# Optimization experiments

Hardware: AMD Instinct MI355X
Metric: run time of the kernel (lower is better)

Reference implementation:

```python
import jax, jax.numpy as jnp
import numpy as np

B, T, D = 8, 1024, 1024

def setup_inputs() -> dict:
    key = jax.random.key(0)
    ks = jax.random.split(key, 9)
    s = D ** -0.5
    return {
        "x": jax.random.normal(ks[0], (B, T, D), dtype=jnp.float32),
        "w_q": jax.random.normal(ks[1], (D, D), dtype=jnp.float32) * s,
        "b_q": jax.random.normal(ks[2], (D,), dtype=jnp.float32) * 0.02,
        "w_k": jax.random.normal(ks[3], (D, D), dtype=jnp.float32) * s,
        "b_k": jax.random.normal(ks[4], (D,), dtype=jnp.float32) * 0.02,
        "w_v": jax.random.normal(ks[5], (D, D), dtype=jnp.float32) * s,
        "b_v": jax.random.normal(ks[6], (D,), dtype=jnp.float32) * 0.02,
        "w_o": jax.random.normal(ks[7], (D, D), dtype=jnp.float32) * s,
        "b_o": jax.random.normal(ks[8], (D,), dtype=jnp.float32) * 0.02,
    }

def reference(x, w_q, b_q, w_k, b_k, w_v, b_v, w_o, b_o):
    d = x.shape[-1]
    scale = jnp.asarray(d, x.dtype) ** -0.5
    q = jnp.einsum('btd,ed->bte', x, w_q) + b_q  # nn.Linear: x @ W^T + b
    k = jnp.einsum('btd,ed->bte', x, w_k) + b_k
    v = jnp.einsum('btd,ed->bte', x, w_v) + b_v
    t = x.shape[1]
    causal = jnp.tril(jnp.ones((t, t), dtype=bool))  # (T, T)
    scores = jnp.einsum('bqd,bkd->bqk', q, k) * scale
    scores = jnp.where(causal, scores, -jnp.inf)
    attn = jax.nn.softmax(scores, axis=-1)  # max-subtraction folded in
    out = jnp.einsum('bqk,bkd->bqd', attn, v)
    return jnp.einsum('btd,ed->bte', out, w_o) + b_o
```

## Files before the change

kernel.cpp:

```cpp
#include <hip/hip_runtime.h>

typedef unsigned short u16;
typedef __attribute__((ext_vector_type(8))) short short8;
typedef __attribute__((ext_vector_type(4))) float f32x4;


__device__ __forceinline__ u16 f2bf(float f) {
  unsigned u = __builtin_bit_cast(unsigned, f);
  u += 0x7fffu + ((u >> 16) & 1u);
  return (u16)(u >> 16);
}

__device__ __forceinline__ void gload16(const void* g, void* l) {
  __builtin_amdgcn_global_load_lds(
      (const __attribute__((address_space(1))) unsigned*)g,
      (__attribute__((address_space(3))) unsigned*)l, 16, 0, 0);
}

__device__ __forceinline__ void gemm_tile(
    const u16* __restrict__ A, int lda,
    const u16* __restrict__ B, int ldb,
    int m0, int n0, int kend,
    char* sA, char* sB, f32x4 acc[4][4])
{
  const int tid  = threadIdx.x;
  const int lane = tid & 63;
  const int wave = tid >> 6;
  const int quad = lane >> 4;
  const int l16  = lane & 15;
  const int wr   = (wave >> 1) << 6;
  const int wc   = (wave & 1) << 6;

  const u16* ga[4]; const u16* gb[4]; int lb[4];
#pragma unroll
  for (int j = 0; j < 4; ++j) {
    const int Lb = j * 256 + wave * 64;
    const int L  = Lb + lane;
    const int r  = L >> 3;
    const int c  = (L & 7) ^ (r & 7);
    lb[j] = Lb * 16;
    ga[j] = A + (size_t)(m0 + r) * lda + c * 8;
    gb[j] = B + (size_t)(n0 + r) * ldb + c * 8;
  }

  for (int kt = 0; kt < kend; kt += 64) {
#pragma unroll
    for (int j = 0; j < 4; ++j) {
      gload16(ga[j], sA + lb[j]);
      gload16(gb[j], sB + lb[j]);
      ga[j] += 64; gb[j] += 64;
    }
    __syncthreads();
#pragma unroll
    for (int kk = 0; kk < 2; ++kk) {
      short8 af[4], bfr[4];
#pragma unroll
      for (int i = 0; i < 4; ++i) {
        const int rm = wr + i * 16 + l16;
        af[i]  = *(const short8*)(sA + rm * 128 + (((kk << 2) + quad) ^ (rm & 7)) * 16);
        const int rn = wc + i * 16 + l16;
        bfr[i] = *(const short8*)(sB + rn * 128 + (((kk << 2) + quad) ^ (rn & 7)) * 16);
      }
#pragma unroll
      for (int i = 0; i < 4; ++i)
#pragma unroll
        for (int j = 0; j < 4; ++j)
          acc[i][j] = __builtin_amdgcn_mfma_f32_16x16x32_bf16(af[i], bfr[j], acc[i][j], 0, 0, 0);
    }
    __syncthreads();
  }
}

__device__ __forceinline__ void gemm_tile_64(
    const u16* __restrict__ A, int lda,
    const u16* __restrict__ B, int ldb,
    int m0, int n0, int kend,
    char* sA, char* sB, f32x4 acc[2][4])
{
  const int tid  = threadIdx.x;
  const int lane = tid & 63;
  const int wave = tid >> 6;
  const int quad = lane >> 4;
  const int l16  = lane & 15;
  const int wr   = (wave >> 1) << 5;
  const int wc   = (wave & 1) << 6;

  const u16* ga[2]; int la[2];
  const u16* gb[4]; int lb[4];
#pragma unroll
  for (int j = 0; j < 2; ++j) {
    const int Lb = j * 256 + wave * 64;
    const int L  = Lb + lane;
    const int r  = L >> 3;
    const int c  = (L & 7) ^ (r & 7);
    la[j] = Lb * 16;
    ga[j] = A + (size_t)(m0 + r) * lda + c * 8;
  }
#pragma unroll
  for (int j = 0; j < 4; ++j) {
    const int Lb = j * 256 + wave * 64;
    const int L  = Lb + lane;
    const int r  = L >> 3;
    const int c  = (L & 7) ^ (r & 7);
    lb[j] = Lb * 16;
    gb[j] = B + (size_t)(n0 + r) * ldb + c * 8;
  }

  for (int kt = 0; kt < kend; kt += 64) {
#pragma unroll
    for (int j = 0; j < 2; ++j) { gload16(ga[j], sA + la[j]); ga[j] += 64; }
#pragma unroll
    for (int j = 0; j < 4; ++j) { gload16(gb[j], sB + lb[j]); gb[j] += 64; }
    __syncthreads();
#pragma unroll
    for (int kk = 0; kk < 2; ++kk) {
      short8 af[2], bfr[4];
#pragma unroll
      for (int i = 0; i < 2; ++i) {
        const int rm = wr + i * 16 + l16;
        af[i] = *(const short8*)(sA + rm * 128 + (((kk << 2) + quad) ^ (rm & 7)) * 16);
      }
#pragma unroll
      for (int j = 0; j < 4; ++j) {
        const int rn = wc + j * 16 + l16;
        bfr[j] = *(const short8*)(sB + rn * 128 + (((kk << 2) + quad) ^ (rn & 7)) * 16);
      }
#pragma unroll
      for (int i = 0; i < 2; ++i)
#pragma unroll
        for (int j = 0; j < 4; ++j)
          acc[i][j] = __builtin_amdgcn_mfma_f32_16x16x32_bf16(af[i], bfr[j], acc[i][j], 0, 0, 0);
    }
    __syncthreads();
  }
}

#define ACC_ZERO4(acc) { _Pragma("unroll") for (int i=0;i<4;++i) \
  _Pragma("unroll") for (int j=0;j<4;++j) \
  _Pragma("unroll") for (int r=0;r<4;++r) acc[i][j][r]=0.f; }
#define ACC_ZERO2(acc) { _Pragma("unroll") for (int i=0;i<2;++i) \
  _Pragma("unroll") for (int j=0;j<4;++j) \
  _Pragma("unroll") for (int r=0;r<4;++r) acc[i][j][r]=0.f; }

__device__ __forceinline__ void store_tile_bf16(
    f32x4 acc[4][4], const float* bias, int nbias0,
    u16* C, int m0, int n0, int ldc, char* smem)
{
  const int tid = threadIdx.x, lane = tid & 63, wave = tid >> 6;
  const int quad = lane >> 4, l16 = lane & 15;
  const int wr = (wave >> 1) << 6, wc = (wave & 1) << 6;
  u16* t = (u16*)smem;
#pragma unroll
  for (int j = 0; j < 4; ++j) {
    const int nn = wc + j * 16 + l16;
    const float bj = bias ? bias[nbias0 + nn] : 0.f;
#pragma unroll
    for (int i = 0; i < 4; ++i) {
      const int mm = wr + i * 16 + quad * 4;
#pragma unroll
      for (int r = 0; r < 4; ++r)
        t[(mm + r) * 136 + nn] = f2bf(acc[i][j][r] + bj);
    }
  }
  __syncthreads();
#pragma unroll
  for (int it = 0; it < 8; ++it) {
    const int L = it * 256 + tid;
    const int mm = L >> 4, cc = L & 15;
    *(uint4*)(C + (size_t)(m0 + mm) * ldc + n0 + cc * 8) =
        *(const uint4*)(t + mm * 136 + cc * 8);
  }
}

__global__ __launch_bounds__(256) void cast_inputs(
    const float* __restrict__ x,  const float* __restrict__ wq,
    const float* __restrict__ wk, const float* __restrict__ wv,
    const float* __restrict__ wo,
    u16* xb, u16* wqb, u16* wkb, u16* wvb, u16* wob, float* rsum)
{
  int b = blockIdx.x;
  if (b < 8) {
    float4 z = {0.f, 0.f, 0.f, 0.f};
    *(float4*)(rsum + (b * 256 + threadIdx.x) * 4) = z;
  }
  const float* src; u16* dst; int base;
  if (b < 4096) { src = x; dst = xb; base = b * 2048; }
  else {
    int r = (b - 4096) >> 9, bb = (b - 4096) & 511;
    base = bb * 2048;
    src = (r == 0) ? wq : (r == 1) ? wk : (r == 2) ? wv : wo;
    dst = (r == 0) ? wqb : (r == 1) ? wkb : (r == 2) ? wvb : wob;
  }
  int i0 = base + threadIdx.x * 8;
  float4 f0 = *(const float4*)(src + i0);
  float4 f1 = *(const float4*)(src + i0 + 4);
  short8 o;
  o[0]=(short)f2bf(f0.x); o[1]=(short)f2bf(f0.y); o[2]=(short)f2bf(f0.z); o[3]=(short)f2bf(f0.w);
  o[4]=(short)f2bf(f1.x); o[5]=(short)f2bf(f1.y); o[6]=(short)f2bf(f1.z); o[7]=(short)f2bf(f1.w);
  *(short8*)(dst + i0) = o;
}

__global__ __launch_bounds__(256) void proj_qkv(
    const u16* __restrict__ xb,
    const u16* __restrict__ wqb, const u16* __restrict__ wkb, const u16* __restrict__ wvb,
    const float* __restrict__ bq, const float* __restrict__ bk, const float* __restrict__ bv,
    u16* q, u16* k, u16* vt)
{
  __shared__ char smem[34816];
  char* sA = smem; char* sB = smem + 16384;
  const int z = blockIdx.z;
  const u16* W = (z == 0) ? wqb : (z == 1) ? wkb : wvb;
  const float* bias = (z == 0) ? bq : (z == 1) ? bk : bv;
  const int id = blockIdx.x + 8 * blockIdx.y;
  const int m0 = ((id & 7) * 8 + (id >> 6)) * 128;
  const int n0 = ((id >> 3) & 7) * 128;

  f32x4 acc[4][4]; ACC_ZERO4(acc);
  gemm_tile(xb, 1024, W, 1024, m0, n0, 1024, sA, sB, acc);

  if (z < 2) {
    store_tile_bf16(acc, bias, n0, (z == 0) ? q : k, m0, n0, 1024, smem);
  } else {
    const int tid = threadIdx.x, lane = tid & 63, wave = tid >> 6;
    const int quad = lane >> 4, l16 = lane & 15;
    const int wr = (wave >> 1) << 6, wc = (wave & 1) << 6;
    u16* t = (u16*)smem;
#pragma unroll
    for (int j = 0; j < 4; ++j) {
      const int nn = wc + j * 16 + l16;
      const float bj = bias[n0 + nn];
#pragma unroll
      for (int i = 0; i < 4; ++i) {
        const int mm = wr + i * 16 + quad * 4;
#pragma unroll
        for (int r = 0; r < 4; ++r)
          t[nn * 136 + mm + r] = f2bf(acc[i][j][r] + bj);
      }
    }
    __syncthreads();
    const int b = m0 >> 10, t0 = m0 & 1023;
#pragma unroll
    for (int it = 0; it < 8; ++it) {
      const int L = it * 256 + tid;
      const int nn = L >> 4, cc = L & 15;
      *(uint4*)(vt + ((size_t)b << 20) + (size_t)(n0 + nn) * 1024 + t0 + cc * 8) =
          *(const uint4*)(t + nn * 136 + cc * 8);
    }
  }
}

__global__ __launch_bounds__(256) void qk_expscores(
    const u16* __restrict__ q, const u16* __restrict__ k,
    u16* __restrict__ probs, float* __restrict__ rowsum)
{
  const int id = blockIdx.x;
  const int b = id / 72, t = id - b * 72;
  int p = (int)((__builtin_sqrtf((float)(4 * t + 1)) - 1.f) * 0.5f);
  while ((p + 1) * (p + 2) <= t) ++p;
  while (p * (p + 1) > t) --p;
  int r0 = t - p * (p + 1);
  const int qi = 2 * p + (r0 >= p + 1);
  const int kb = (r0 >= p + 1) ? r0 - (p + 1) : r0;

  __shared__ char smem[24576];
  char* sA = smem; char* sB = smem + 8192;
  const u16* A = q + ((size_t)b << 20);
  const u16* B = k + ((size_t)b << 20);
  const int m0 = qi * 64, n0 = kb * 128;

  f32x4 acc[2][4]; ACC_ZERO2(acc);
  gemm_tile_64(A, 1024, B, 1024, m0, n0, 1024, sA, sB, acc);

  const int tid = threadIdx.x, lane = tid & 63, wave = tid >> 6;
  const int quad = lane >> 4, l16 = lane & 15;
  const int wr = (wave >> 1) << 5, wc = (wave & 1) << 6;
  const bool diag = (kb == (qi >> 1));

  float part[2][4];
#pragma unroll
  for (int i = 0; i < 2; ++i)
#pragma unroll
    for (int r = 0; r < 4; ++r) part[i][r] = 0.f;

  u16* tl = (u16*)smem;
#pragma unroll
  for (int j = 0; j < 4; ++j) {
    const int nn = wc + j * 16 + l16;
#pragma unroll
    for (int i = 0; i < 2; ++i) {
      const int mm = wr + i * 16 + quad * 4;
#pragma unroll
      for (int r = 0; r < 4; ++r) {
        float e = __expf(acc[i][j][r] * 0.03125f);
        if (diag && (n0 + nn) > (m0 + mm + r)) e = 0.f;
        part[i][r] += e;
        tl[(mm + r) * 136 + nn] = f2bf(e);
      }
    }
  }
  float* rs = rowsum + b * 1024 + m0;
#pragma unroll
  for (int i = 0; i < 2; ++i)
#pragma unroll
    for (int r = 0; r < 4; ++r) {
      float v = part[i][r];
      v += __shfl_xor(v, 1); v += __shfl_xor(v, 2);
      v += __shfl_xor(v, 4); v += __shfl_xor(v, 8);
      if (l16 == 0) atomicAdd(rs + wr + i * 16 + quad * 4 + r, v);
    }
  __syncthreads();
  u16* C = probs + ((size_t)b << 20);
#pragma unroll
  for (int it = 0; it < 4; ++it) {
    const int L = it * 256 + tid;
    const int mm = L >> 4, cc = L & 15;
    *(uint4*)(C + (size_t)(m0 + mm) * 1024 + n0 + cc * 8) =
        *(const uint4*)(tl + mm * 136 + cc * 8);
  }
}

__global__ __launch_bounds__(256) void pv_gemm(
    const u16* __restrict__ probs, const u16* __restrict__ vt,
    const float* __restrict__ rowsum, u16* __restrict__ o)
{
  const int id = blockIdx.x;
  const int b = id & 7, nb = (id >> 3) & 7, qi = 15 - (id >> 6);
  __shared__ char smem[24576];
  char* sA = smem; char* sB = smem + 8192;
  const u16* A = probs + ((size_t)b << 20);
  const u16* B = vt + ((size_t)b << 20);
  const int m0 = qi * 64, n0 = nb * 128;
  const int kend = (qi + 1) * 64;

  f32x4 acc[2][4]; ACC_ZERO2(acc);
  gemm_tile_64(A, 1024, B, 1024, m0, n0, kend, sA, sB, acc);

  const int tid = threadIdx.x, lane = tid & 63, wave = tid >> 6;
  const int quad = lane >> 4, l16 = lane & 15;
  const int wr = (wave >> 1) << 5, wc = (wave & 1) << 6;
  const float* rs = rowsum + b * 1024 + m0;
  u16* tl = (u16*)smem;
#pragma unroll
  for (int i = 0; i < 2; ++i)
#pragma unroll
    for (int r = 0; r < 4; ++r) {
      const int mm = wr + i * 16 + quad * 4 + r;
      const float inv = 1.0f / rs[mm];
#pragma unroll
      for (int j = 0; j < 4; ++j)
        tl[mm * 136 + wc + j * 16 + l16] = f2bf(acc[i][j][r] * inv);
    }
  __syncthreads();
  u16* C = o + ((size_t)b << 20);
#pragma unroll
  for (int it = 0; it < 4; ++it) {
    const int L = it * 256 + tid;
    const int mm = L >> 4, cc = L & 15;
    *(uint4*)(C + (size_t)(m0 + mm) * 1024 + n0 + cc * 8) =
        *(const uint4*)(tl + mm * 136 + cc * 8);
  }
}

__global__ __launch_bounds__(256) void proj_o(
    const u16* __restrict__ ob, const u16* __restrict__ wob,
    const float* __restrict__ bo, float* __restrict__ out)
{
  __shared__ char smem[34816];
  char* sA = smem; char* sB = smem + 8192;
  const int id = blockIdx.x;
  const int m0 = ((id & 7) * 16 + (id >> 6)) * 64;
  const int n0 = ((id >> 3) & 7) * 128;
  f32x4 acc[2][4]; ACC_ZERO2(acc);
  gemm_tile_64(ob, 1024, wob, 1024, m0, n0, 1024, sA, sB, acc);

  const int tid = threadIdx.x, lane = tid & 63, wave = tid >> 6;
  const int quad = lane >> 4, l16 = lane & 15;
  const int wr = (wave >> 1) << 5, wc = (wave & 1) << 6;
  float* tf = (float*)smem;
#pragma unroll
  for (int j = 0; j < 4; ++j) {
    const int nn = wc + j * 16 + l16;
    const float bj = bo[n0 + nn];
#pragma unroll
    for (int i = 0; i < 2; ++i)
#pragma unroll
      for (int r = 0; r < 4; ++r)
        tf[(wr + i * 16 + quad * 4 + r) * 132 + nn] = acc[i][j][r] + bj;
  }
  __syncthreads();
#pragma unroll
  for (int it = 0; it < 8; ++it) {
    const int L = it * 256 + tid;
    const int mm = L >> 5, cc = L & 31;
    *(float4*)(out + (size_t)(m0 + mm) * 1024 + n0 + cc * 4) =
        *(const float4*)(tf + mm * 132 + cc * 4);
  }
}

extern "C" void kernel_launch(void* const* d_in, const int* in_sizes, int n_in,
                              void* d_out, int out_size, void* d_ws, size_t ws_size,
                              hipStream_t stream) {
  const float* x  = (const float*)d_in[0];
  const float* wq = (const float*)d_in[1];
  const float* bq = (const float*)d_in[2];
  const float* wk = (const float*)d_in[3];
  const float* bk = (const float*)d_in[4];
  const float* wv = (const float*)d_in[5];
  const float* bv = (const float*)d_in[6];
  const float* wo = (const float*)d_in[7];
  const float* bo = (const float*)d_in[8];
  float* out = (float*)d_out;

  char* ws = (char*)d_ws;
  const size_t MB = 1u << 20;
  u16*  xb  = (u16*)(ws);
  u16*  wqb = (u16*)(ws + 16*MB);
  u16*  wkb = (u16*)(ws + 18*MB);
  u16*  wvb = (u16*)(ws + 20*MB);
  u16*  wob = (u16*)(ws + 22*MB);
  u16*  qb  = (u16*)(ws + 24*MB);
  u16*  kb  = (u16*)(ws + 40*MB);
  u16*  vtb = (u16*)(ws + 56*MB);
  u16*  pr  = (u16*)(ws + 72*MB);
  float* rsum = (float*)(ws + 88*MB);

  cast_inputs<<<6144, 256, 0, stream>>>(x, wq, wk, wv, wo, xb, wqb, wkb, wvb, wob, rsum);
  proj_qkv<<<dim3(8, 64, 3), 256, 0, stream>>>(xb, wqb, wkb, wvb, bq, bk, bv, qb, kb, vtb);
  qk_expscores<<<576, 256, 0, stream>>>(qb, kb, pr, rsum);
  pv_gemm<<<1024, 256, 0, stream>>>(pr, vtb, rsum, xb );
  proj_o<<<1024, 256, 0, stream>>>(xb, wob, bo, out);
}
```

Baseline: 230.3 us.

## Use triple-buffered 256x128 GEMM tiles with 512 threads for projections

Replaces the single-buffered 128x128 (QKV) and 64x128 (output) projection GEMMs with a 256x128 tile kernel of 8 waves. It uses a three-stage LDS ring filled by direct global-to-LDS loads, split half-tile MFMA phases, explicit waitcnt/barrier scheduling and raised wave priority during MFMA bursts. The goal is to hide global load latency behind matrix math and to reuse data more per block. In exchange it needs 144 KB of LDS per block, which limits occupancy to one block per CU. Grids shrink to 256 blocks per weight matrix, so load balance now depends on matching the CU count.

```diff
diff --git a/kernel.cpp b/kernel.cpp
--- a/kernel.cpp
+++ b/kernel.cpp
@@ -17,57 +17,165 @@
       (__attribute__((address_space(3))) unsigned*)l, 16, 0, 0);
 }
 
-__device__ __forceinline__ void gemm_tile(
-    const u16* __restrict__ A, int lda,
-    const u16* __restrict__ B, int ldb,
-    int m0, int n0, int kend,
-    char* sA, char* sB, f32x4 acc[4][4])
+
+#define QTILE(CUR, NXT, DOSTAGE, VM)                                         \
+  {                                                                          \
+    char* cA = sA0 + (CUR) * 32768;                                          \
+    char* cB = sB0 + (CUR) * 16384;                                          \
+    short8 bf[2][4], af[2][2];                                               \
+                         \
+    _Pragma("unroll") for (int kk = 0; kk < 2; ++kk)                         \
+      _Pragma("unroll") for (int j = 0; j < 4; ++j) {                        \
+        const int rn = wc + j * 16 + l16;                                    \
+        bf[kk][j] = *(const short8*)(cB + rn * 128 + (((kk << 2) + quad) ^ (rn & 7)) * 16); \
+      }                                                                      \
+    _Pragma("unroll") for (int kk = 0; kk < 2; ++kk)                         \
+      _Pragma("unroll") for (int i = 0; i < 2; ++i) {                        \
+        const int rm = wr + i * 16 + l16;                                    \
+        af[kk][i] = *(const short8*)(cA + rm * 128 + (((kk << 2) + quad) ^ (rm & 7)) * 16); \
+      }                                                                      \
+    if (DOSTAGE) {                                                           \
+      char* dA = sA0 + (NXT) * 32768;                                        \
+      _Pragma("unroll") for (int j = 0; j < 3; ++j) { gload16(ga[j], dA + la[j]); ga[j] += 64; } \
+    }                                                                        \
+    asm volatile("" ::: "memory");                                           \
+    __builtin_amdgcn_s_barrier();                                            \
+    asm volatile("s_waitcnt lgkmcnt(0)" ::: "memory");                       \
+    __builtin_amdgcn_sched_barrier(0);                                       \
+    __builtin_amdgcn_s_setprio(1);                                           \
+    _Pragma("unroll") for (int kk = 0; kk < 2; ++kk)                         \
+      _Pragma("unroll") for (int i = 0; i < 2; ++i)                          \
+        _Pragma("unroll") for (int j = 0; j < 4; ++j)                        \
+          acc[i][j] = __builtin_amdgcn_mfma_f32_16x16x32_bf16(af[kk][i], bf[kk][j], acc[i][j], 0, 0, 0); \
+    __builtin_amdgcn_s_setprio(0);                                           \
+    asm volatile("" ::: "memory");                                           \
+    __builtin_amdgcn_s_barrier();                                            \
+    asm volatile("" ::: "memory");                                           \
+                                \
+    _Pragma("unroll") for (int kk = 0; kk < 2; ++kk)                         \
+      _Pragma("unroll") for (int i = 0; i < 2; ++i) {                        \
+        const int rm = wr + 32 + i * 16 + l16;                               \
+        af[kk][i] = *(const short8*)(cA + rm * 128 + (((kk << 2) + quad) ^ (rm & 7)) * 16); \
+      }                                                                      \
+    if (DOSTAGE) {                                                           \
+      char* dA = sA0 + (NXT) * 32768;                                        \
+      char* dB = sB0 + (NXT) * 16384;                                        \
+      gload16(ga[3], dA + la[3]); ga[3] += 64;                               \
+      _Pragma("unroll") for (int j = 0; j < 2; ++j) { gload16(gb[j], dB + lb[j]); gb[j] += 64; } \
+    }                                                                        \
+    asm volatile("s_waitcnt vmcnt(" #VM ")" ::: "memory");                   \
+    asm volatile("" ::: "memory");                                           \
+    __builtin_amdgcn_s_barrier();                                            \
+    asm volatile("s_waitcnt lgkmcnt(0)" ::: "memory");                       \
+    __builtin_amdgcn_sched_barrier(0);                                       \
+    __builtin_amdgcn_s_setprio(1);                                           \
+    _Pragma("unroll") for (int kk = 0; kk < 2; ++kk)                         \
+      _Pragma("unroll") for (int i = 0; i < 2; ++i)                          \
+        _Pragma("unroll") for (int j = 0; j < 4; ++j)                        \
+          acc[2 + i][j] = __builtin_amdgcn_mfma_f32_16x16x32_bf16(af[kk][i], bf[kk][j], acc[2 + i][j], 0, 0, 0); \
+    __builtin_amdgcn_s_setprio(0);                                           \
+    asm volatile("" ::: "memory");                                           \
+    __builtin_amdgcn_s_barrier();                                            \
+    asm volatile("" ::: "memory");                                           \
+  }
+
+__device__ __forceinline__ void gemm_256x128(
+    const u16* __restrict__ A, const u16* __restrict__ B,
+    int m0, int n0, char* smem, f32x4 acc[4][4])
 {
   const int tid  = threadIdx.x;
   const int lane = tid & 63;
-  const int wave = tid >> 6;
   const int quad = lane >> 4;
   const int l16  = lane & 15;
+  const int wave = tid >> 6;
   const int wr   = (wave >> 1) << 6;
   const int wc   = (wave & 1) << 6;
 
-  const u16* ga[4]; const u16* gb[4]; int lb[4];
+  const u16* ga[4]; int la[4];
+  const u16* gb[2]; int lb[2];
 #pragma unroll
   for (int j = 0; j < 4; ++j) {
-    const int Lb = j * 256 + wave * 64;
-    const int L  = Lb + lane;
-    const int r  = L >> 3;
-    const int c  = (L & 7) ^ (r & 7);
-    lb[j] = Lb * 16;
-    ga[j] = A + (size_t)(m0 + r) * lda + c * 8;
-    gb[j] = B + (size_t)(n0 + r) * ldb + c * 8;
-  }
-
-  for (int kt = 0; kt < kend; kt += 64) {
-#pragma unroll
-    for (int j = 0; j < 4; ++j) {
-      gload16(ga[j], sA + lb[j]);
-      gload16(gb[j], sB + lb[j]);
-      ga[j] += 64; gb[j] += 64;
-    }
-    __syncthreads();
-#pragma unroll
-    for (int kk = 0; kk < 2; ++kk) {
-      short8 af[4], bfr[4];
-#pragma unroll
-      for (int i = 0; i < 4; ++i) {
-        const int rm = wr + i * 16 + l16;
-        af[i]  = *(const short8*)(sA + rm * 128 + (((kk << 2) + quad) ^ (rm & 7)) * 16);
-        const int rn = wc + i * 16 + l16;
-        bfr[i] = *(const short8*)(sB + rn * 128 + (((kk << 2) + quad) ^ (rn & 7)) * 16);
-      }
-#pragma unroll
-      for (int i = 0; i < 4; ++i)
-#pragma unroll
-        for (int j = 0; j < 4; ++j)
-          acc[i][j] = __builtin_amdgcn_mfma_f32_16x16x32_bf16(af[i], bfr[j], acc[i][j], 0, 0, 0);
-    }
-    __syncthreads();
+    const int L = j * 512 + tid;
+    const int r = L >> 3;
+    const int c = (L & 7) ^ (r & 7);
+    la[j] = L * 16;
+    ga[j] = A + (size_t)(m0 + r) * 1024 + c * 8;
+  }
+#pragma unroll
+  for (int j = 0; j < 2; ++j) {
+    const int L = j * 512 + tid;
+    const int r = L >> 3;
+    const int c = (L & 7) ^ (r & 7);
+    lb[j] = L * 16;
+    gb[j] = B + (size_t)(n0 + r) * 1024 + c * 8;
+  }
+  char* const sA0 = smem;
+  char* const sB0 = smem + 98304;
+
+  {
+    char* dA = sA0; char* dB = sB0;
+#pragma unroll
+    for (int j = 0; j < 4; ++j) { gload16(ga[j], dA + la[j]); ga[j] += 64; }
+#pragma unroll
+    for (int j = 0; j < 2; ++j) { gload16(gb[j], dB + lb[j]); gb[j] += 64; }
+  }
+  {
+    char* dA = sA0 + 32768; char* dB = sB0 + 16384;
+#pragma unroll
+    for (int j = 0; j < 4; ++j) { gload16(ga[j], dA + la[j]); ga[j] += 64; }
+#pragma unroll
+    for (int j = 0; j < 2; ++j) { gload16(gb[j], dB + lb[j]); gb[j] += 64; }
+  }
+  asm volatile("s_waitcnt vmcnt(6)" ::: "memory");
+  __builtin_amdgcn_s_barrier();
+  asm volatile("" ::: "memory");
+
+  int cur = 0;
+#pragma unroll 1
+  for (int t = 0; t < 14; ++t) {
+    int nxt = cur + 2; if (nxt >= 3) nxt -= 3;
+    QTILE(cur, nxt, true, 6);
+    cur = (cur + 1 == 3) ? 0 : cur + 1;
+  }
+  QTILE(cur, 0, false, 0);
+  cur = (cur + 1 == 3) ? 0 : cur + 1;
+  QTILE(cur, 0, false, 0);
+}
+
+#define ACC_ZERO4(acc) { _Pragma("unroll") for (int i=0;i<4;++i) \
+  _Pragma("unroll") for (int j=0;j<4;++j) \
+  _Pragma("unroll") for (int r=0;r<4;++r) acc[i][j][r]=0.f; }
+#define ACC_ZERO2(acc) { _Pragma("unroll") for (int i=0;i<2;++i) \
+  _Pragma("unroll") for (int j=0;j<4;++j) \
+  _Pragma("unroll") for (int r=0;r<4;++r) acc[i][j][r]=0.f; }
+
+__device__ __forceinline__ void store256x128_bf16(
+    f32x4 acc[4][4], const float* bias, int n0,
+    u16* C, int m0, char* smem)
+{
+  const int tid = threadIdx.x, lane = tid & 63, wave = tid >> 6;
+  const int quad = lane >> 4, l16 = lane & 15;
+  const int wr = (wave >> 1) << 6, wc = (wave & 1) << 6;
+  u16* t = (u16*)smem;
+#pragma unroll
+  for (int j = 0; j < 4; ++j) {
+    const int nn = wc + j * 16 + l16;
+    const float bj = bias[n0 + nn];
+#pragma unroll
+    for (int i = 0; i < 4; ++i) {
+      const int mm = wr + i * 16 + quad * 4;
+#pragma unroll
+      for (int r = 0; r < 4; ++r)
+        t[(mm + r) * 136 + nn] = f2bf(acc[i][j][r] + bj);
+    }
+  }
+  __syncthreads();
+#pragma unroll
+  for (int it = 0; it < 8; ++it) {
+    const int L = it * 512 + tid;
+    const int mm = L >> 4, cc = L & 15;
+    *(uint4*)(C + (size_t)(m0 + mm) * 1024 + n0 + cc * 8) =
+        *(const uint4*)(t + mm * 136 + cc * 8);
   }
 }
 
@@ -135,43 +243,6 @@
   }
 }
 
-#define ACC_ZERO4(acc) { _Pragma("unroll") for (int i=0;i<4;++i) \
-  _Pragma("unroll") for (int j=0;j<4;++j) \
-  _Pragma("unroll") for (int r=0;r<4;++r) acc[i][j][r]=0.f; }
-#define ACC_ZERO2(acc) { _Pragma("unroll") for (int i=0;i<2;++i) \
-  _Pragma("unroll") for (int j=0;j<4;++j) \
-  _Pragma("unroll") for (int r=0;r<4;++r) acc[i][j][r]=0.f; }
-
-__device__ __forceinline__ void store_tile_bf16(
-    f32x4 acc[4][4], const float* bias, int nbias0,
-    u16* C, int m0, int n0, int ldc, char* smem)
-{
-  const int tid = threadIdx.x, lane = tid & 63, wave = tid >> 6;
-  const int quad = lane >> 4, l16 = lane & 15;
-  const int wr = (wave >> 1) << 6, wc = (wave & 1) << 6;
-  u16* t = (u16*)smem;
-#pragma unroll
-  for (int j = 0; j < 4; ++j) {
-    const int nn = wc + j * 16 + l16;
-    const float bj = bias ? bias[nbias0 + nn] : 0.f;
-#pragma unroll
-    for (int i = 0; i < 4; ++i) {
-      const int mm = wr + i * 16 + quad * 4;
-#pragma unroll
-      for (int r = 0; r < 4; ++r)
-        t[(mm + r) * 136 + nn] = f2bf(acc[i][j][r] + bj);
-    }
-  }
-  __syncthreads();
-#pragma unroll
-  for (int it = 0; it < 8; ++it) {
-    const int L = it * 256 + tid;
-    const int mm = L >> 4, cc = L & 15;
-    *(uint4*)(C + (size_t)(m0 + mm) * ldc + n0 + cc * 8) =
-        *(const uint4*)(t + mm * 136 + cc * 8);
-  }
-}
-
 __global__ __launch_bounds__(256) void cast_inputs(
     const float* __restrict__ x,  const float* __restrict__ wq,
     const float* __restrict__ wk, const float* __restrict__ wv,
@@ -200,26 +271,25 @@
   *(short8*)(dst + i0) = o;
 }
 
-__global__ __launch_bounds__(256) void proj_qkv(
+__global__ __launch_bounds__(512, 2) void proj_qkv(
     const u16* __restrict__ xb,
     const u16* __restrict__ wqb, const u16* __restrict__ wkb, const u16* __restrict__ wvb,
     const float* __restrict__ bq, const float* __restrict__ bk, const float* __restrict__ bv,
     u16* q, u16* k, u16* vt)
 {
-  __shared__ char smem[34816];
-  char* sA = smem; char* sB = smem + 16384;
-  const int z = blockIdx.z;
+  __shared__ char smem[147456];
+  const int z = blockIdx.y;
   const u16* W = (z == 0) ? wqb : (z == 1) ? wkb : wvb;
   const float* bias = (z == 0) ? bq : (z == 1) ? bk : bv;
-  const int id = blockIdx.x + 8 * blockIdx.y;
-  const int m0 = ((id & 7) * 8 + (id >> 6)) * 128;
-  const int n0 = ((id >> 3) & 7) * 128;
+  const int id = blockIdx.x;
+  const int m0 = ((id & 7) * 4 + ((id >> 3) & 3)) * 256;
+  const int n0 = (id >> 5) * 128;
 
   f32x4 acc[4][4]; ACC_ZERO4(acc);
-  gemm_tile(xb, 1024, W, 1024, m0, n0, 1024, sA, sB, acc);
+  gemm_256x128(xb, W, m0, n0, smem, acc);
 
   if (z < 2) {
-    store_tile_bf16(acc, bias, n0, (z == 0) ? q : k, m0, n0, 1024, smem);
+    store256x128_bf16(acc, bias, n0, (z == 0) ? q : k, m0, smem);
   } else {
     const int tid = threadIdx.x, lane = tid & 63, wave = tid >> 6;
     const int quad = lane >> 4, l16 = lane & 15;
@@ -234,17 +304,17 @@
         const int mm = wr + i * 16 + quad * 4;
 #pragma unroll
         for (int r = 0; r < 4; ++r)
-          t[nn * 136 + mm + r] = f2bf(acc[i][j][r] + bj);
+          t[nn * 264 + mm + r] = f2bf(acc[i][j][r] + bj);
       }
     }
     __syncthreads();
     const int b = m0 >> 10, t0 = m0 & 1023;
 #pragma unroll
     for (int it = 0; it < 8; ++it) {
-      const int L = it * 256 + tid;
-      const int nn = L >> 4, cc = L & 15;
+      const int L = it * 512 + tid;
+      const int nn = L >> 5, cc = L & 31;
       *(uint4*)(vt + ((size_t)b << 20) + (size_t)(n0 + nn) * 1024 + t0 + cc * 8) =
-          *(const uint4*)(t + nn * 136 + cc * 8);
+          *(const uint4*)(t + nn * 264 + cc * 8);
     }
   }
 }
@@ -361,36 +431,35 @@
   }
 }
 
-__global__ __launch_bounds__(256) void proj_o(
+__global__ __launch_bounds__(512, 2) void proj_o(
     const u16* __restrict__ ob, const u16* __restrict__ wob,
     const float* __restrict__ bo, float* __restrict__ out)
 {
-  __shared__ char smem[34816];
-  char* sA = smem; char* sB = smem + 8192;
+  __shared__ char smem[147456];
   const int id = blockIdx.x;
-  const int m0 = ((id & 7) * 16 + (id >> 6)) * 64;
-  const int n0 = ((id >> 3) & 7) * 128;
-  f32x4 acc[2][4]; ACC_ZERO2(acc);
-  gemm_tile_64(ob, 1024, wob, 1024, m0, n0, 1024, sA, sB, acc);
+  const int m0 = ((id & 7) * 4 + ((id >> 3) & 3)) * 256;
+  const int n0 = (id >> 5) * 128;
+  f32x4 acc[4][4]; ACC_ZERO4(acc);
+  gemm_256x128(ob, wob, m0, n0, smem, acc);
 
   const int tid = threadIdx.x, lane = tid & 63, wave = tid >> 6;
   const int quad = lane >> 4, l16 = lane & 15;
-  const int wr = (wave >> 1) << 5, wc = (wave & 1) << 6;
+  const int wr = (wave >> 1) << 6, wc = (wave & 1) << 6;
   float* tf = (float*)smem;
 #pragma unroll
   for (int j = 0; j < 4; ++j) {
     const int nn = wc + j * 16 + l16;
     const float bj = bo[n0 + nn];
 #pragma unroll
-    for (int i = 0; i < 2; ++i)
+    for (int i = 0; i < 4; ++i)
 #pragma unroll
       for (int r = 0; r < 4; ++r)
         tf[(wr + i * 16 + quad * 4 + r) * 132 + nn] = acc[i][j][r] + bj;
   }
   __syncthreads();
 #pragma unroll
-  for (int it = 0; it < 8; ++it) {
-    const int L = it * 256 + tid;
+  for (int it = 0; it < 16; ++it) {
+    const int L = it * 512 + tid;
     const int mm = L >> 5, cc = L & 31;
     *(float4*)(out + (size_t)(m0 + mm) * 1024 + n0 + cc * 4) =
         *(const float4*)(tf + mm * 132 + cc * 4);
@@ -425,8 +494,8 @@
   float* rsum = (float*)(ws + 88*MB);
 
   cast_inputs<<<6144, 256, 0, stream>>>(x, wq, wk, wv, wo, xb, wqb, wkb, wvb, wob, rsum);
-  proj_qkv<<<dim3(8, 64, 3), 256, 0, stream>>>(xb, wqb, wkb, wvb, bq, bk, bv, qb, kb, vtb);
+  proj_qkv<<<dim3(256, 3), 512, 0, stream>>>(xb, wqb, wkb, wvb, bq, bk, bv, qb, kb, vtb);
   qk_expscores<<<576, 256, 0, stream>>>(qb, kb, pr, rsum);
   pv_gemm<<<1024, 256, 0, stream>>>(pr, vtb, rsum, xb );
-  proj_o<<<1024, 256, 0, stream>>>(xb, wob, bo, out);
-}
+  proj_o<<<256, 512, 0, stream>>>(xb, wob, bo, out);
+}
```

Result: no change. 234.1 us (+1.7%).
